# Kernel optimization log

Hardware: AMD Instinct MI355X
Metric: run time of the kernel (lower is better)

The kernel has to match this reference:

```python
import jax, jax.numpy as jnp
import numpy as np

N_ATOMS = 4096
N_EDGES = 131072
NUM_BASIS = 8
CUTOFF = 6.0
EMBED = 64      # atom embedding dim
HID = 128       # hidden channel width
SH_DIM = 9      # l=0,1,2 spherical harmonics
TP_IN = HID * SH_DIM  # 1152
N_HEADS = 4
HEAD_DIM = HID // N_HEADS


def _spherical_harmonics(vec):
    # vec: [E,3] -> [E,9] matching the torch SphericalHarmonics (l=0,1,2)
    r = jnp.linalg.norm(vec, axis=-1, keepdims=True) + 1e-8
    u = vec / r
    x, y, z = u[:, 0], u[:, 1], u[:, 2]
    l0 = jnp.ones_like(x)[:, None]
    l1 = jnp.stack([y, z, x], axis=-1)
    l2 = jnp.stack([3.0 * z * z - 1.0, x * z, y * z, x * y, x * x - y * y], axis=-1)
    return jnp.concatenate([l0, l1, l2], axis=-1)


def _rbf(d):
    # bessel RBF with cosine cutoff, d: [E] -> [E, NUM_BASIS]
    freqs = jnp.arange(1, NUM_BASIS + 1, dtype=d.dtype) * (np.pi / CUTOFF)
    cut = 0.5 * (jnp.cos(d * (np.pi / CUTOFF)) + 1.0) * (d < CUTOFF).astype(d.dtype)
    rbf = jnp.sin(d[:, None] * freqs) / d[:, None]
    return rbf * cut[:, None]


def _mace_block(atomic_numbers, edge_index, edge_vectors, edge_lengths,
                atom_embed, rad_w1, rad_b1, rad_w2, rad_b2, tp_w, tp_b,
                msg_w1, msg_b1, msg_w2, msg_b2,
                attn_w_in, attn_b_in, attn_w_out, attn_b_out,
                gate_w, gate_b, out_w, out_b):
    n_atoms = atom_embed.shape[0] if False else atomic_numbers.shape[0]
    node = atom_embed[atomic_numbers]                      # [N,64] gather
    sh = _spherical_harmonics(edge_vectors)                # [E,9]
    rbf = _rbf(edge_lengths)                               # [E,8]
    rad = jax.nn.silu(rbf @ rad_w1 + rad_b1)
    rad = jax.nn.silu(rad @ rad_w2 + rad_b2)               # [E,128]
    # per-l outer products radial x sh_l, flattened channel-major, concatenated
    slices = [(0, 1), (1, 4), (4, 9)]
    msgs = jnp.concatenate(
        [(rad[:, :, None] * sh[:, None, s:e]).reshape(rad.shape[0], -1) for s, e in slices],
        axis=-1)                                           # [E,1152]
    edge_msg = msgs @ tp_w + tp_b                          # [E,128]
    dst = edge_index[1]
    agg = jax.ops.segment_sum(edge_msg, dst, num_segments=n_atoms)  # [N,128] scatter-add
    combined = jnp.concatenate([node, agg], axis=-1)       # [N,192]
    upd = jax.nn.silu(combined @ msg_w1 + msg_b1) @ msg_w2 + msg_b2  # [N,128]
    # multi-head self-attention over all atoms (batch of 1)
    qkv = upd @ attn_w_in.T + attn_b_in                    # [N,384]
    q, k, v = jnp.split(qkv, 3, axis=-1)
    q = q.reshape(-1, N_HEADS, HEAD_DIM)
    k = k.reshape(-1, N_HEADS, HEAD_DIM)
    v = v.reshape(-1, N_HEADS, HEAD_DIM)
    scores = jnp.einsum('nhd,mhd->hnm', q, k) / np.sqrt(HEAD_DIM)
    attn = jax.nn.softmax(scores, axis=-1)
    att = jnp.einsum('hnm,mhd->nhd', attn, v).reshape(-1, HID)
    att = att @ attn_w_out.T + attn_b_out                  # [N,128]
    gate = jax.nn.sigmoid(upd @ gate_w + gate_b)
    out = gate * att + (1.0 - gate) * upd
    return out @ out_w + out_b                             # [N,128]


def setup_inputs() -> dict:
    key = jax.random.key(0)
    ks = jax.random.split(key, 20)
    def w(k, shape, s=0.05):
        return jax.random.normal(k, shape, dtype=jnp.float32) * s
    return {
        'atomic_numbers': jax.random.randint(ks[0], (N_ATOMS,), 0, 100),
        'positions': jax.random.normal(ks[1], (N_ATOMS, 3), dtype=jnp.float32),
        'edge_index': jax.random.randint(ks[2], (2, N_EDGES), 0, N_ATOMS),
        'edge_vectors': jax.random.normal(ks[3], (N_EDGES, 3), dtype=jnp.float32),
        'edge_lengths': jax.random.uniform(ks[4], (N_EDGES,), dtype=jnp.float32, minval=0.5, maxval=5.9),
        'atom_embed': w(ks[5], (100, EMBED), 1.0),
        'rad_w1': w(ks[6], (NUM_BASIS, 64)), 'rad_b1': jnp.zeros((64,), jnp.float32),
        'rad_w2': w(ks[7], (64, HID)), 'rad_b2': jnp.zeros((HID,), jnp.float32),
        'tp_w': w(ks[8], (TP_IN, HID)), 'tp_b': jnp.zeros((HID,), jnp.float32),
        'msg_w1': w(ks[9], (EMBED + HID, HID)), 'msg_b1': jnp.zeros((HID,), jnp.float32),
        'msg_w2': w(ks[10], (HID, HID)), 'msg_b2': jnp.zeros((HID,), jnp.float32),
        'attn_w_in': w(ks[11], (3 * HID, HID)), 'attn_b_in': jnp.zeros((3 * HID,), jnp.float32),
        'attn_w_out': w(ks[12], (HID, HID)), 'attn_b_out': jnp.zeros((HID,), jnp.float32),
        'gate_w': w(ks[13], (HID, HID)), 'gate_b': jnp.zeros((HID,), jnp.float32),
        'out_w': w(ks[14], (HID, HID)), 'out_b': jnp.zeros((HID,), jnp.float32),
    }


def reference(atomic_numbers, positions, edge_index, edge_vectors, edge_lengths,
              atom_embed, rad_w1, rad_b1, rad_w2, rad_b2, tp_w, tp_b,
              msg_w1, msg_b1, msg_w2, msg_b2,
              attn_w_in, attn_b_in, attn_w_out, attn_b_out,
              gate_w, gate_b, out_w, out_b):
    # positions is accepted (as in the torch signature) but unused by the block math
    del positions
    return _mace_block(atomic_numbers, edge_index, edge_vectors, edge_lengths,
                       atom_embed, rad_w1, rad_b1, rad_w2, rad_b2, tp_w, tp_b,
                       msg_w1, msg_b1, msg_w2, msg_b2,
                       attn_w_in, attn_b_in, attn_w_out, attn_b_out,
                       gate_w, gate_b, out_w, out_b)
```

## Files before the change

### kernel.cpp

```cpp
#include <hip/hip_runtime.h>
#include <math.h>

#define N_ATOMS 4096
#define N_EDGES 131072
#define PI6 0.52359877559829887f
#define CAP 128

typedef __attribute__((ext_vector_type(8))) short bf16x8;
typedef __attribute__((ext_vector_type(4))) float f32x4;

#define MFMA(A,B,C) __builtin_amdgcn_mfma_f32_16x16x32_bf16((A),(B),(C),0,0,0)

__device__ __forceinline__ float silu_f(float x){ return x / (1.f + __expf(-x)); }
__device__ __forceinline__ float sigmoid_f(float x){ return 1.f / (1.f + __expf(-x)); }
__device__ __forceinline__ unsigned int f2bf(float f){
  unsigned int u = __float_as_uint(f);
  return (u + 0x7FFFu + ((u>>16)&1u)) >> 16;
}
__device__ __forceinline__ bf16x8 ld8(const unsigned short* p){
  union { unsigned int u[4]; bf16x8 v; } r;
  const unsigned int* q = (const unsigned int*)p;
  r.u[0]=q[0]; r.u[1]=q[1]; r.u[2]=q[2]; r.u[3]=q[3];
  return r.v;
}
__device__ __forceinline__ void split_store(float v, unsigned short* ph, unsigned short* pl){
  unsigned int hb = f2bf(v);
  *ph = (unsigned short)hb;
  *pl = (unsigned short)f2bf(v - __uint_as_float(hb<<16));
}

__global__ __launch_bounds__(256) void prep_kernel(
  const float* __restrict__ attn_w_out, const float* __restrict__ rad_w2,
  const float* __restrict__ tp_w, const float* __restrict__ msg_w1,
  const float* __restrict__ msg_w2, const float* __restrict__ attn_w_in,
  float* __restrict__ wt_out, int* __restrict__ cursor,
  unsigned short* __restrict__ w2t_h, unsigned short* __restrict__ w2t_l,
  unsigned short* __restrict__ tpwT_h, unsigned short* __restrict__ tpwT_l,
  unsigned short* __restrict__ w1T_h, unsigned short* __restrict__ w1T_l,
  unsigned short* __restrict__ w2T_h, unsigned short* __restrict__ w2T_l,
  unsigned short* __restrict__ awin_h, unsigned short* __restrict__ awin_l)
{
  int idx = blockIdx.x*256 + threadIdx.x;
  if (idx < 4096) cursor[idx] = 0;
  if (idx < 16384){
    int i = idx>>7, k = idx&127;
    wt_out[k*128+i] = attn_w_out[idx];
  } else if (idx < 24576){
    int j = idx - 16384; int k = j>>7, c = j&127;
    split_store(rad_w2[k*128+c], &w2t_h[c*64+k], &w2t_l[c*64+k]);
  } else if (idx < 172032){
    int j = idx - 24576; int col = j&127, kk = j>>7;
    int jj = kk>>7, c = kk&127;
    int r = (jj==0)? c : (jj<4 ? 128 + c*3 + (jj-1) : 512 + c*5 + (jj-4));
    split_store(tp_w[r*128+col], &tpwT_h[col*1152+kk], &tpwT_l[col*1152+kk]);
  } else if (idx < 196608){
    int j = idx - 172032; int col = j&127, k = j>>7;
    split_store(msg_w1[k*128+col], &w1T_h[col*192+k], &w1T_l[col*192+k]);
  } else if (idx < 212992){
    int j = idx - 196608; int col = j&127, k = j>>7;
    split_store(msg_w2[k*128+col], &w2T_h[col*128+k], &w2T_l[col*128+k]);
  } else if (idx < 262144){
    int j = idx - 212992;
    split_store(attn_w_in[j], &awin_h[j], &awin_l[j]);
  }
}

__global__ __launch_bounds__(256) void bucket_kernel(
  const int* __restrict__ edge_index, int* __restrict__ cursor, int* __restrict__ edge_slot)
{
  int e = blockIdx.x*256 + threadIdx.x;
  if (e < N_EDGES){
    int d = edge_index[N_EDGES + e];
    int pos = atomicAdd(&cursor[d], 1);
    if (pos < CAP) edge_slot[d*CAP + pos] = e;
  }
}

__global__ __launch_bounds__(512) void edge_F_kernel(
  const float* __restrict__ edge_vectors, const float* __restrict__ edge_lengths,
  const float* __restrict__ rad_w1, const float* __restrict__ rad_b1,
  const unsigned short* __restrict__ w2t_h, const unsigned short* __restrict__ w2t_l,
  const float* __restrict__ rad_b2,
  const int* __restrict__ cursor, const int* __restrict__ edge_slot,
  unsigned short* __restrict__ Fh, unsigned short* __restrict__ Fl)
{
  const int tid = threadIdx.x;
  const int w = tid >> 6, lane = tid & 63;
  const int l15 = lane & 15, lg = lane >> 4;
  const int wm = w >> 2, wn2 = w & 3;

  __shared__ unsigned short W1h[64][36],  W1l[64][36];
  __shared__ unsigned short RBh[32][36],  RBl[32][36];
  __shared__ unsigned short SHh[16][36],  SHl[16][36];
  __shared__ unsigned short R1h[32][72],  R1l[32][72];
  __shared__ unsigned short R2h[128][36], R2l[128][36];

  bf16x8 WBh[2][2], WBl[2][2];
  #pragma unroll
  for (int nt=0; nt<2; nt++){
    int row = (wn2*2+nt)*16 + l15;
    WBh[nt][0] = ld8(&w2t_h[row*64 + lg*8]);
    WBh[nt][1] = ld8(&w2t_h[row*64 + 32 + lg*8]);
    WBl[nt][0] = ld8(&w2t_l[row*64 + lg*8]);
    WBl[nt][1] = ld8(&w2t_l[row*64 + 32 + lg*8]);
  }

  for (int i = tid; i < 2048; i += 512){
    int c = i >> 5, k = i & 31;
    float v = (k < 8) ? rad_w1[k*64 + c] : 0.f;
    split_store(v, &W1h[c][k], &W1l[c][k]);
  }
  for (int i = tid; i < 32*36; i += 512){ RBh[i/36][i%36]=0; RBl[i/36][i%36]=0; }
  for (int i = tid; i < 16*36; i += 512){ SHh[i/36][i%36]=0; SHl[i/36][i%36]=0; }

  const float b1v  = rad_b1[wn2*16 + l15];
  const float b2c0 = rad_b2[wn2*32 + l15];
  const float b2c1 = rad_b2[wn2*32 + 16 + l15];

  __syncthreads();

  for (int aa = 0; aa < 4; ++aa){
    const int a = blockIdx.x*4 + aa;
    const int deg = min(cursor[a], CAP);
    const int base = a*CAP;
    f32x4 facc = {0.f,0.f,0.f,0.f};

    for (int t0 = 0; t0 < deg; t0 += 32){
      if (tid < 256){
        int e8 = tid >> 3, k = tid & 7;
        int idx = t0 + e8;
        int eid = edge_slot[base + (idx < deg ? idx : 0)];
        float d = edge_lengths[eid];
        float cut = 0.5f*(__cosf(d*PI6)+1.f)*(d<6.f?1.f:0.f);
        float rb = __sinf(d*((float)(k+1)*PI6))/d*cut;
        split_store(rb, &RBh[e8][k], &RBl[e8][k]);
      } else {
        int e8 = (tid-256) >> 3, u = tid & 7;
        int idx = t0 + e8;
        bool val = idx < deg;
        int eid = edge_slot[base + (val ? idx : 0)];
        float vx = edge_vectors[eid*3], vy = edge_vectors[eid*3+1], vz = edge_vectors[eid*3+2];
        float rn = sqrtf(vx*vx+vy*vy+vz*vz) + 1e-8f;
        float x = vx/rn, y = vy/rn, z = vz/rn;
        float sv;
        switch(u){
          case 0: sv = 1.f; break;
          case 1: sv = y; break;
          case 2: sv = z; break;
          case 3: sv = x; break;
          case 4: sv = 3.f*z*z-1.f; break;
          case 5: sv = x*z; break;
          case 6: sv = y*z; break;
          default: sv = x*y; break;
        }
        if (!val) sv = 0.f;
        split_store(sv, &SHh[u][e8], &SHl[u][e8]);
        if (u == 0){
          float s8 = val ? (x*x - y*y) : 0.f;
          split_store(s8, &SHh[8][e8], &SHl[8][e8]);
        }
      }
      __syncthreads();

      {
        bf16x8 Ah = ld8(&RBh[wm*16 + l15][lg*8]);
        bf16x8 Al = ld8(&RBl[wm*16 + l15][lg*8]);
        bf16x8 Bh = ld8(&W1h[wn2*16 + l15][lg*8]);
        bf16x8 Bl = ld8(&W1l[wn2*16 + l15][lg*8]);
        f32x4 z = {0.f,0.f,0.f,0.f};
        z = MFMA(Ah,Bl,z); z = MFMA(Al,Bh,z); z = MFMA(Ah,Bh,z);
        #pragma unroll
        for (int r=0;r<4;r++){
          int e8 = wm*16 + lg*4 + r;
          int c  = wn2*16 + l15;
          float v = silu_f(z[r] + b1v);
          split_store(v, &R1h[e8][c], &R1l[e8][c]);
        }
      }
      __syncthreads();

      {
        bf16x8 Ah0 = ld8(&R1h[wm*16+l15][lg*8]);
        bf16x8 Ah1 = ld8(&R1h[wm*16+l15][32+lg*8]);
        bf16x8 Al0 = ld8(&R1l[wm*16+l15][lg*8]);
        bf16x8 Al1 = ld8(&R1l[wm*16+l15][32+lg*8]);
        #pragma unroll
        for (int nt=0; nt<2; nt++){
          int c16 = wn2*2 + nt;
          f32x4 z = {0.f,0.f,0.f,0.f};
          z = MFMA(Al0,WBh[nt][0],z); z = MFMA(Al1,WBh[nt][1],z);
          z = MFMA(Ah0,WBl[nt][0],z); z = MFMA(Ah1,WBl[nt][1],z);
          z = MFMA(Ah0,WBh[nt][0],z); z = MFMA(Ah1,WBh[nt][1],z);
          float bb = nt ? b2c1 : b2c0;
          #pragma unroll
          for (int r=0;r<4;r++){
            int e8 = wm*16 + lg*4 + r;
            int c  = c16*16 + l15;
            float v = silu_f(z[r] + bb);
            split_store(v, &R2h[c][e8], &R2l[c][e8]);
          }
        }
      }
      __syncthreads();

      {
        bf16x8 Ah = ld8(&R2h[w*16+l15][lg*8]);
        bf16x8 Al = ld8(&R2l[w*16+l15][lg*8]);
        bf16x8 Bh = ld8(&SHh[l15][lg*8]);
        bf16x8 Bl = ld8(&SHl[l15][lg*8]);
        facc = MFMA(Ah,Bl,facc);
        facc = MFMA(Al,Bh,facc);
        facc = MFMA(Ah,Bh,facc);
      }
      __syncthreads();
    }

    if (l15 < 9){
      #pragma unroll
      for (int r=0;r<4;r++){
        int c = w*16 + lg*4 + r;
        size_t o = (size_t)l15*(N_ATOMS*128) + (size_t)a*128 + c;
        split_store(facc[r], &Fh[o], &Fl[o]);
      }
    }
  }
}

__global__ __launch_bounds__(512) void node_kernel(
  const int* __restrict__ atomic_numbers, const float* __restrict__ atom_embed,
  const unsigned short* __restrict__ Fh, const unsigned short* __restrict__ Fl,
  const unsigned short* __restrict__ tpwT_h, const unsigned short* __restrict__ tpwT_l,
  const float* __restrict__ tp_b, const int* __restrict__ cursor,
  const unsigned short* __restrict__ w1T_h, const unsigned short* __restrict__ w1T_l,
  const float* __restrict__ msg_b1,
  const unsigned short* __restrict__ w2T_h, const unsigned short* __restrict__ w2T_l,
  const float* __restrict__ msg_b2,
  const unsigned short* __restrict__ awin_h, const unsigned short* __restrict__ awin_l,
  const float* __restrict__ attn_b_in,
  float* __restrict__ upd_out,
  unsigned short* __restrict__ Qbf, unsigned short* __restrict__ Kbf,
  unsigned short* __restrict__ Vtb)
{
  const int a0 = blockIdx.x*16, tid = threadIdx.x;
  const int w = tid>>6, lane = tid&63, l15 = lane&15, lg = lane>>4;

  __shared__ unsigned short Ch[16][200], Cl[16][200];
  __shared__ unsigned short Hh[16][136], Hl[16][136];
  __shared__ unsigned short Uh[16][136], Ul[16][136];

  for (int i=tid; i<1024; i+=512){
    int a16=i>>6, k=i&63;
    float v = atom_embed[atomic_numbers[a0+a16]*64+k];
    split_store(v, &Ch[a16][k], &Cl[a16][k]);
  }

  {
    f32x4 z = {0.f,0.f,0.f,0.f};
    for (int ch=0; ch<36; ch++){
      int k0=ch*32, j=k0>>7, c0=k0&127;
      size_t aoff = (size_t)j*(N_ATOMS*128) + (size_t)(a0+l15)*128 + c0 + lg*8;
      bf16x8 Ah=ld8(Fh+aoff), Al=ld8(Fl+aoff);
      size_t boff = (size_t)(w*16+l15)*1152 + k0 + lg*8;
      bf16x8 Bh=ld8(tpwT_h+boff), Bl=ld8(tpwT_l+boff);
      z = MFMA(Ah,Bl,z); z = MFMA(Al,Bh,z); z = MFMA(Ah,Bh,z);
    }
    int col = w*16+l15;
    float tb = tp_b[col];
    #pragma unroll
    for (int r=0;r<4;r++){
      int row = lg*4+r, arow = a0+row;
      float deg = (float)cursor[arow];
      float v = z[r] + tb*deg;
      split_store(v, &Ch[row][64+col], &Cl[row][64+col]);
    }
  }
  __syncthreads();

  {
    f32x4 z = {0.f,0.f,0.f,0.f};
    #pragma unroll
    for (int ch=0; ch<6; ch++){
      int k0=ch*32;
      bf16x8 Ah=ld8(&Ch[l15][k0+lg*8]), Al=ld8(&Cl[l15][k0+lg*8]);
      size_t boff=(size_t)(w*16+l15)*192 + k0 + lg*8;
      bf16x8 Bh=ld8(w1T_h+boff), Bl=ld8(w1T_l+boff);
      z = MFMA(Ah,Bl,z); z = MFMA(Al,Bh,z); z = MFMA(Ah,Bh,z);
    }
    int col = w*16+l15;
    float mb = msg_b1[col];
    #pragma unroll
    for (int r=0;r<4;r++){
      int row = lg*4+r;
      float v = silu_f(z[r]+mb);
      split_store(v, &Hh[row][col], &Hl[row][col]);
    }
  }
  __syncthreads();

  {
    f32x4 z = {0.f,0.f,0.f,0.f};
    #pragma unroll
    for (int ch=0; ch<4; ch++){
      int k0=ch*32;
      bf16x8 Ah=ld8(&Hh[l15][k0+lg*8]), Al=ld8(&Hl[l15][k0+lg*8]);
      size_t boff=(size_t)(w*16+l15)*128 + k0 + lg*8;
      bf16x8 Bh=ld8(w2T_h+boff), Bl=ld8(w2T_l+boff);
      z = MFMA(Ah,Bl,z); z = MFMA(Al,Bh,z); z = MFMA(Ah,Bh,z);
    }
    int col = w*16+l15;
    float mb = msg_b2[col];
    #pragma unroll
    for (int r=0;r<4;r++){
      int row = lg*4+r;
      float v = z[r]+mb;
      upd_out[(size_t)(a0+row)*128 + col] = v;
      split_store(v, &Uh[row][col], &Ul[row][col]);
    }
  }
  __syncthreads();

  #pragma unroll
  for (int t3=0; t3<3; t3++){
    f32x4 z = {0.f,0.f,0.f,0.f};
    int col = (w*3+t3)*16 + l15;
    #pragma unroll
    for (int ch=0; ch<4; ch++){
      int k0=ch*32;
      bf16x8 Ah=ld8(&Uh[l15][k0+lg*8]), Al=ld8(&Ul[l15][k0+lg*8]);
      size_t boff=(size_t)col*128 + k0 + lg*8;
      bf16x8 Bh=ld8(awin_h+boff), Bl=ld8(awin_l+boff);
      z = MFMA(Ah,Bl,z); z = MFMA(Al,Bh,z); z = MFMA(Ah,Bh,z);
    }
    float ab = attn_b_in[col];
    int p = col>>7, hh = (col>>5)&3, dd = col&31;
    #pragma unroll
    for (int r=0;r<4;r++){
      int row = a0 + lg*4 + r;
      float v = z[r]+ab;
      if (p==0)      Qbf[(size_t)hh*131072 + (size_t)row*32 + dd] =
                       (unsigned short)f2bf(v*0.17677669529663687f);
      else if (p==1) Kbf[(size_t)hh*131072 + (size_t)row*32 + dd] = (unsigned short)f2bf(v);
      else           Vtb[(size_t)hh*131072 + (size_t)dd*4096 + row] = (unsigned short)f2bf(v);
    }
  }
}

__global__ __launch_bounds__(512) void attn_kernel(
  const unsigned short* __restrict__ Qbf, const unsigned short* __restrict__ Kbf,
  const unsigned short* __restrict__ Vtb, float* __restrict__ att)
{
  const int tid = threadIdx.x;
  const int w = tid>>6, lane = tid&63, l15 = lane&15, lg = lane>>4;
  const int qjl = w>>2, ks = w&3;
  const int qj = blockIdx.x*2 + qjl;
  const int h = qj >> 8, qt = qj & 255;

  __shared__ unsigned short Ps[8][16][72];
  __shared__ float MBo[2][4][16][32];
  __shared__ float MBm[2][4][16];
  __shared__ float MBs[2][4][16];

  const unsigned short* Kb = Kbf + (size_t)h*131072;
  const unsigned short* Vb = Vtb + (size_t)h*131072;

  bf16x8 bQ = ld8(&Qbf[(size_t)h*131072 + (size_t)(qt*16+l15)*32 + lg*8]);

  float m = -3e38f, su = 0.f;
  f32x4 oacc[2] = {{0.f,0.f,0.f,0.f},{0.f,0.f,0.f,0.f}};

  for (int kt = ks*16; kt < ks*16 + 16; ++kt){
    const int k0 = kt*64;
    f32x4 s[4];
    #pragma unroll
    for (int n=0;n<4;n++){
      bf16x8 aK = ld8(&Kb[(size_t)(k0+n*16+l15)*32 + lg*8]);
      f32x4 z = {0.f,0.f,0.f,0.f};
      s[n] = MFMA(aK, bQ, z);
    }
    float tmax = s[0][0];
    #pragma unroll
    for (int n=0;n<4;n++)
      #pragma unroll
      for (int r=0;r<4;r++) tmax = fmaxf(tmax, s[n][r]);
    tmax = fmaxf(tmax, __shfl_xor(tmax,16,64));
    tmax = fmaxf(tmax, __shfl_xor(tmax,32,64));
    float mn = fmaxf(m, tmax);
    float csc = __expf(m - mn);
    m = mn;
    float psum = 0.f;
    unsigned int* prow = (unsigned int*)&Ps[w][l15][0];
    #pragma unroll
    for (int n=0;n<4;n++){
      float p0=__expf(s[n][0]-mn), p1=__expf(s[n][1]-mn);
      float p2=__expf(s[n][2]-mn), p3=__expf(s[n][3]-mn);
      psum += (p0+p1)+(p2+p3);
      prow[n*8+lg*2]   = f2bf(p0) | (f2bf(p1)<<16);
      prow[n*8+lg*2+1] = f2bf(p2) | (f2bf(p3)<<16);
    }
    psum += __shfl_xor(psum,16,64);
    psum += __shfl_xor(psum,32,64);
    su = su*csc + psum;
    float cr[4];
    #pragma unroll
    for (int r=0;r<4;r++) cr[r] = __shfl(csc, lg*4+r, 64);
    #pragma unroll
    for (int nd=0;nd<2;nd++)
      #pragma unroll
      for (int r=0;r<4;r++) oacc[nd][r] *= cr[r];
    __asm__ volatile("s_waitcnt lgkmcnt(0)" ::: "memory");
    #pragma unroll
    for (int kc=0;kc<2;kc++){
      bf16x8 aP = ld8(&Ps[w][l15][kc*32 + lg*8]);
      #pragma unroll
      for (int nd=0;nd<2;nd++){
        bf16x8 bV = ld8(&Vb[(size_t)(nd*16+l15)*4096 + k0 + kc*32 + lg*8]);
        oacc[nd] = MFMA(aP, bV, oacc[nd]);
      }
    }
  }

  if (lg==0){ MBm[qjl][ks][l15]=m; MBs[qjl][ks][l15]=su; }
  #pragma unroll
  for (int nd=0;nd<2;nd++)
    #pragma unroll
    for (int r=0;r<4;r++) MBo[qjl][ks][lg*4+r][nd*16+l15] = oacc[nd][r];
  __syncthreads();

  for (int idx = tid; idx < 1024; idx += 512){
    int qq = idx>>9, q = (idx>>5)&15, d = idx&31;
    float m0=MBm[qq][0][q], m1=MBm[qq][1][q], m2=MBm[qq][2][q], m3=MBm[qq][3][q];
    float mf = fmaxf(fmaxf(m0,m1), fmaxf(m2,m3));
    float c0=__expf(m0-mf), c1=__expf(m1-mf), c2=__expf(m2-mf), c3=__expf(m3-mf);
    float st = MBs[qq][0][q]*c0 + MBs[qq][1][q]*c1 + MBs[qq][2][q]*c2 + MBs[qq][3][q]*c3;
    float o  = MBo[qq][0][q][d]*c0 + MBo[qq][1][q][d]*c1 + MBo[qq][2][q][d]*c2 + MBo[qq][3][q][d]*c3;
    int qj2 = blockIdx.x*2 + qq;
    int hh = qj2>>8, qrow = (qj2&255)*16 + q;
    att[(size_t)qrow*128 + hh*32 + d] = o/st;
  }
}

__global__ __launch_bounds__(512) void final_kernel(
  const float* __restrict__ att, const float* __restrict__ upd,
  const float* __restrict__ wt_out, const float* __restrict__ attn_b_out,
  const float* __restrict__ gate_w, const float* __restrict__ gate_b,
  const float* __restrict__ out_w, const float* __restrict__ out_b,
  float* __restrict__ out)
{
  const int a0 = blockIdx.x*8, tid = threadIdx.x;
  const int g = tid >> 7, o = tid & 127;
  __shared__ float att_s[8][128], upd_s[8][128], tmps[8][128];
  for (int i=tid; i<1024; i+=512){
    int a8 = i>>7, k = i&127;
    att_s[a8][k] = att[(a0+a8)*128+k];
    upd_s[a8][k] = upd[(a0+a8)*128+k];
  }
  __syncthreads();
  const int aA = 2*g, aB = 2*g+1;
  float a2A = attn_b_out[o], a2B = a2A;
  float gA = gate_b[o], gB = gA;
  for (int k=0;k<128;k++){
    float wa = wt_out[k*128+o];
    float wg = gate_w[k*128+o];
    a2A += att_s[aA][k]*wa; a2B += att_s[aB][k]*wa;
    gA  += upd_s[aA][k]*wg; gB  += upd_s[aB][k]*wg;
  }
  gA = sigmoid_f(gA); gB = sigmoid_f(gB);
  tmps[aA][o] = gA*a2A + (1.f-gA)*upd_s[aA][o];
  tmps[aB][o] = gB*a2B + (1.f-gB)*upd_s[aB][o];
  __syncthreads();
  float ouA = out_b[o], ouB = ouA;
  for (int k=0;k<128;k++){
    float w = out_w[k*128+o];
    ouA += tmps[aA][k]*w; ouB += tmps[aB][k]*w;
  }
  out[(a0+aA)*128+o] = ouA;
  out[(a0+aB)*128+o] = ouB;
}

extern "C" void kernel_launch(void* const* d_in, const int* in_sizes, int n_in,
                              void* d_out, int out_size, void* d_ws, size_t ws_size,
                              hipStream_t stream){
  const int*   atomic_numbers = (const int*)  d_in[0];
  const int*   edge_index     = (const int*)  d_in[2];
  const float* edge_vectors   = (const float*)d_in[3];
  const float* edge_lengths   = (const float*)d_in[4];
  const float* atom_embed     = (const float*)d_in[5];
  const float* rad_w1 = (const float*)d_in[6];
  const float* rad_b1 = (const float*)d_in[7];
  const float* rad_w2 = (const float*)d_in[8];
  const float* rad_b2 = (const float*)d_in[9];
  const float* tp_w   = (const float*)d_in[10];
  const float* tp_b   = (const float*)d_in[11];
  const float* msg_w1 = (const float*)d_in[12];
  const float* msg_b1 = (const float*)d_in[13];
  const float* msg_w2 = (const float*)d_in[14];
  const float* msg_b2 = (const float*)d_in[15];
  const float* attn_w_in  = (const float*)d_in[16];
  const float* attn_b_in  = (const float*)d_in[17];
  const float* attn_w_out = (const float*)d_in[18];
  const float* attn_b_out = (const float*)d_in[19];
  const float* gate_w = (const float*)d_in[20];
  const float* gate_b = (const float*)d_in[21];
  const float* out_w  = (const float*)d_in[22];
  const float* out_b  = (const float*)d_in[23];

  char* ws = (char*)d_ws;
  int* cursor    = (int*)(ws);
  int* edge_slot = (int*)(ws + 16384);
  float* wt_out  = (float*)(ws + 2113536);
  unsigned short* w2t_h  = (unsigned short*)(ws + 2179072);
  unsigned short* w2t_l  = (unsigned short*)(ws + 2195456);
  unsigned short* tpwT_h = (unsigned short*)(ws + 2211840);
  unsigned short* tpwT_l = (unsigned short*)(ws + 2506752);
  unsigned short* w1T_h  = (unsigned short*)(ws + 2801664);
  unsigned short* w1T_l  = (unsigned short*)(ws + 2850816);
  unsigned short* w2T_h  = (unsigned short*)(ws + 2899968);
  unsigned short* w2T_l  = (unsigned short*)(ws + 2932736);
  unsigned short* awin_h = (unsigned short*)(ws + 2965504);
  unsigned short* awin_l = (unsigned short*)(ws + 3063808);
  unsigned short* Fbf_h  = (unsigned short*)(ws + 3162112);
  unsigned short* Fbf_l  = (unsigned short*)(ws + 12599296);
  float* att     = (float*)(ws + 3162112);
  float* upd     = (float*)(ws + 22036480);
  unsigned short* Qbf = (unsigned short*)(ws + 24133632);
  unsigned short* Kbf = (unsigned short*)(ws + 25182208);
  unsigned short* Vtb = (unsigned short*)(ws + 26230784);

  prep_kernel<<<1024, 256, 0, stream>>>(attn_w_out, rad_w2, tp_w, msg_w1, msg_w2, attn_w_in,
      wt_out, cursor, w2t_h, w2t_l, tpwT_h, tpwT_l, w1T_h, w1T_l, w2T_h, w2T_l, awin_h, awin_l);
  bucket_kernel<<<(N_EDGES+255)/256, 256, 0, stream>>>(edge_index, cursor, edge_slot);
  edge_F_kernel<<<N_ATOMS/4, 512, 0, stream>>>(edge_vectors, edge_lengths,
      rad_w1, rad_b1, w2t_h, w2t_l, rad_b2, cursor, edge_slot, Fbf_h, Fbf_l);
  node_kernel<<<N_ATOMS/16, 512, 0, stream>>>(atomic_numbers, atom_embed,
      Fbf_h, Fbf_l, tpwT_h, tpwT_l, tp_b, cursor,
      w1T_h, w1T_l, msg_b1, w2T_h, w2T_l, msg_b2, awin_h, awin_l, attn_b_in,
      upd, Qbf, Kbf, Vtb);
  attn_kernel<<<512, 512, 0, stream>>>(Qbf, Kbf, Vtb, att);
  final_kernel<<<N_ATOMS/8, 512, 0, stream>>>(att, upd, wt_out, attn_b_out,
      gate_w, gate_b, out_w, out_b, (float*)d_out);
}
```

Before: 191.9 us.

## Process 64-edge tiles and keep layer-2 output per-wave to drop a barrier

The edge tile grows from 32 to 64 edges, and every thread now computes both RBF and spherical-harmonic values instead of splitting that work across halves. The layer-2 GEMM is transposed so each wave owns 16 output channels and writes them to a private per-wave LDS buffer. The SH contraction then reads that buffer after only a wave-local waitcnt, which removes one block-wide __syncthreads per tile and halves the number of tile iterations. In exchange the kernel uses more LDS and registers, and atoms with low degree waste more work on padding rows.

```diff
diff --git a/kernel.cpp b/kernel.cpp
--- a/kernel.cpp
+++ b/kernel.cpp
@@ -87,35 +87,36 @@
   const int tid = threadIdx.x;
   const int w = tid >> 6, lane = tid & 63;
   const int l15 = lane & 15, lg = lane >> 4;
-  const int wm = w >> 2, wn2 = w & 3;
+  const int m = w >> 1, nh = w & 1;
 
   __shared__ unsigned short W1h[64][36],  W1l[64][36];
-  __shared__ unsigned short RBh[32][36],  RBl[32][36];
-  __shared__ unsigned short SHh[16][36],  SHl[16][36];
-  __shared__ unsigned short R1h[32][72],  R1l[32][72];
-  __shared__ unsigned short R2h[128][36], R2l[128][36];
-
-  bf16x8 WBh[2][2], WBl[2][2];
-  #pragma unroll
-  for (int nt=0; nt<2; nt++){
-    int row = (wn2*2+nt)*16 + l15;
-    WBh[nt][0] = ld8(&w2t_h[row*64 + lg*8]);
-    WBh[nt][1] = ld8(&w2t_h[row*64 + 32 + lg*8]);
-    WBl[nt][0] = ld8(&w2t_l[row*64 + lg*8]);
-    WBl[nt][1] = ld8(&w2t_l[row*64 + 32 + lg*8]);
-  }
-
-  for (int i = tid; i < 2048; i += 512){
-    int c = i >> 5, k = i & 31;
+  __shared__ unsigned short RBh[64][36],  RBl[64][36];
+  __shared__ unsigned short SHh[16][72],  SHl[16][72];
+  __shared__ unsigned short R1h[64][66],  R1l[64][66];
+  __shared__ unsigned short R2wh[8][16][34], R2wl[8][16][34];
+
+  bf16x8 WAh[2], WAl[2];
+  {
+    int c = w*16 + l15;
+    WAh[0] = ld8(&w2t_h[c*64 + lg*8]);
+    WAh[1] = ld8(&w2t_h[c*64 + 32 + lg*8]);
+    WAl[0] = ld8(&w2t_l[c*64 + lg*8]);
+    WAl[1] = ld8(&w2t_l[c*64 + 32 + lg*8]);
+  }
+
+  for (int i = tid; i < 64*36; i += 512){
+    int c = i/36, k = i%36;
     float v = (k < 8) ? rad_w1[k*64 + c] : 0.f;
     split_store(v, &W1h[c][k], &W1l[c][k]);
-  }
-  for (int i = tid; i < 32*36; i += 512){ RBh[i/36][i%36]=0; RBl[i/36][i%36]=0; }
-  for (int i = tid; i < 16*36; i += 512){ SHh[i/36][i%36]=0; SHl[i/36][i%36]=0; }
-
-  const float b1v  = rad_b1[wn2*16 + l15];
-  const float b2c0 = rad_b2[wn2*32 + l15];
-  const float b2c1 = rad_b2[wn2*32 + 16 + l15];
+    RBh[c][k]=0; RBl[c][k]=0;
+  }
+  for (int i = tid; i < 16*72; i += 512){ SHh[i/72][i%72]=0; SHl[i/72][i%72]=0; }
+
+  const float b1A = rad_b1[nh*32 + l15];
+  const float b1B = rad_b1[nh*32 + 16 + l15];
+  float b2r[4];
+  #pragma unroll
+  for (int r=0;r<4;r++) b2r[r] = rad_b2[w*16 + lg*4 + r];
 
   __syncthreads();
 
@@ -125,20 +126,16 @@
     const int base = a*CAP;
     f32x4 facc = {0.f,0.f,0.f,0.f};
 
-    for (int t0 = 0; t0 < deg; t0 += 32){
-      if (tid < 256){
-        int e8 = tid >> 3, k = tid & 7;
-        int idx = t0 + e8;
-        int eid = edge_slot[base + (idx < deg ? idx : 0)];
-        float d = edge_lengths[eid];
-        float cut = 0.5f*(__cosf(d*PI6)+1.f)*(d<6.f?1.f:0.f);
-        float rb = __sinf(d*((float)(k+1)*PI6))/d*cut;
-        split_store(rb, &RBh[e8][k], &RBl[e8][k]);
-      } else {
-        int e8 = (tid-256) >> 3, u = tid & 7;
+    for (int t0 = 0; t0 < deg; t0 += 64){
+      {
+        int e8 = tid >> 3, u = tid & 7;
         int idx = t0 + e8;
         bool val = idx < deg;
         int eid = edge_slot[base + (val ? idx : 0)];
+        float d = edge_lengths[eid];
+        float cut = 0.5f*(__cosf(d*PI6)+1.f)*(d<6.f?1.f:0.f);
+        float rb = __sinf(d*((float)(u+1)*PI6))/d*cut;
+        split_store(rb, &RBh[e8][u], &RBl[e8][u]);
         float vx = edge_vectors[eid*3], vy = edge_vectors[eid*3+1], vz = edge_vectors[eid*3+2];
         float rn = sqrtf(vx*vx+vy*vy+vz*vz) + 1e-8f;
         float x = vx/rn, y = vy/rn, z = vz/rn;
@@ -163,54 +160,56 @@
       __syncthreads();
 
       {
-        bf16x8 Ah = ld8(&RBh[wm*16 + l15][lg*8]);
-        bf16x8 Al = ld8(&RBl[wm*16 + l15][lg*8]);
-        bf16x8 Bh = ld8(&W1h[wn2*16 + l15][lg*8]);
-        bf16x8 Bl = ld8(&W1l[wn2*16 + l15][lg*8]);
-        f32x4 z = {0.f,0.f,0.f,0.f};
-        z = MFMA(Ah,Bl,z); z = MFMA(Al,Bh,z); z = MFMA(Ah,Bh,z);
-        #pragma unroll
-        for (int r=0;r<4;r++){
-          int e8 = wm*16 + lg*4 + r;
-          int c  = wn2*16 + l15;
-          float v = silu_f(z[r] + b1v);
-          split_store(v, &R1h[e8][c], &R1l[e8][c]);
-        }
-      }
-      __syncthreads();
-
-      {
-        bf16x8 Ah0 = ld8(&R1h[wm*16+l15][lg*8]);
-        bf16x8 Ah1 = ld8(&R1h[wm*16+l15][32+lg*8]);
-        bf16x8 Al0 = ld8(&R1l[wm*16+l15][lg*8]);
-        bf16x8 Al1 = ld8(&R1l[wm*16+l15][32+lg*8]);
+        bf16x8 Ah = ld8(&RBh[m*16 + l15][lg*8]);
+        bf16x8 Al = ld8(&RBl[m*16 + l15][lg*8]);
         #pragma unroll
         for (int nt=0; nt<2; nt++){
-          int c16 = wn2*2 + nt;
+          int c = nh*32 + nt*16 + l15;
+          bf16x8 Bh = ld8(&W1h[c][lg*8]);
+          bf16x8 Bl = ld8(&W1l[c][lg*8]);
           f32x4 z = {0.f,0.f,0.f,0.f};
-          z = MFMA(Al0,WBh[nt][0],z); z = MFMA(Al1,WBh[nt][1],z);
-          z = MFMA(Ah0,WBl[nt][0],z); z = MFMA(Ah1,WBl[nt][1],z);
-          z = MFMA(Ah0,WBh[nt][0],z); z = MFMA(Ah1,WBh[nt][1],z);
-          float bb = nt ? b2c1 : b2c0;
+          z = MFMA(Ah,Bl,z); z = MFMA(Al,Bh,z); z = MFMA(Ah,Bh,z);
+          float bb = nt ? b1B : b1A;
           #pragma unroll
           for (int r=0;r<4;r++){
-            int e8 = wm*16 + lg*4 + r;
-            int c  = c16*16 + l15;
+            int e8 = m*16 + lg*4 + r;
+            int cc = nh*32 + nt*16 + l15;
             float v = silu_f(z[r] + bb);
-            split_store(v, &R2h[c][e8], &R2l[c][e8]);
+            split_store(v, &R1h[e8][cc], &R1l[e8][cc]);
           }
         }
       }
       __syncthreads();
 
-      {
-        bf16x8 Ah = ld8(&R2h[w*16+l15][lg*8]);
-        bf16x8 Al = ld8(&R2l[w*16+l15][lg*8]);
-        bf16x8 Bh = ld8(&SHh[l15][lg*8]);
-        bf16x8 Bl = ld8(&SHl[l15][lg*8]);
-        facc = MFMA(Ah,Bl,facc);
-        facc = MFMA(Al,Bh,facc);
-        facc = MFMA(Ah,Bh,facc);
+      #pragma unroll
+      for (int eh=0; eh<2; eh++){
+        #pragma unroll
+        for (int nt2=0; nt2<2; nt2++){
+          int et = eh*2 + nt2;
+          bf16x8 Bh0 = ld8(&R1h[et*16+l15][lg*8]);
+          bf16x8 Bh1 = ld8(&R1h[et*16+l15][32+lg*8]);
+          bf16x8 Bl0 = ld8(&R1l[et*16+l15][lg*8]);
+          bf16x8 Bl1 = ld8(&R1l[et*16+l15][32+lg*8]);
+          f32x4 z = {0.f,0.f,0.f,0.f};
+          z = MFMA(WAl[0],Bh0,z); z = MFMA(WAl[1],Bh1,z);
+          z = MFMA(WAh[0],Bl0,z); z = MFMA(WAh[1],Bl1,z);
+          z = MFMA(WAh[0],Bh0,z); z = MFMA(WAh[1],Bh1,z);
+          #pragma unroll
+          for (int r=0;r<4;r++){
+            float v = silu_f(z[r] + b2r[r]);
+            split_store(v, &R2wh[w][lg*4+r][nt2*16+l15], &R2wl[w][lg*4+r][nt2*16+l15]);
+          }
+        }
+        __asm__ volatile("s_waitcnt lgkmcnt(0)" ::: "memory");
+        {
+          bf16x8 Ah = ld8(&R2wh[w][l15][lg*8]);
+          bf16x8 Al = ld8(&R2wl[w][l15][lg*8]);
+          bf16x8 Bh = ld8(&SHh[l15][eh*32 + lg*8]);
+          bf16x8 Bl = ld8(&SHl[l15][eh*32 + lg*8]);
+          facc = MFMA(Ah,Bl,facc);
+          facc = MFMA(Al,Bh,facc);
+          facc = MFMA(Ah,Bh,facc);
+        }
       }
       __syncthreads();
     }
```

New measurement: 192.4 us. No clear change (+0.2%).

## Make second radial layer wave-local to drop a block barrier

Applied to the files above, without the earlier changes.

Each wave now computes its own 16-channel slice of the second radial MLP layer across all 32 edges, with W2 transposed as the A operand. The result goes to a per-wave LDS buffer, so the following tensor-product MFMA only needs a wave-local lgkmcnt wait instead of a block-wide __syncthreads. Padded RBF rows are zeroed explicitly so that invalid edges contribute nothing. The scheme relies on wave-local LDS ordering and on the sched_barrier being placed correctly.

```diff
diff --git a/kernel.cpp b/kernel.cpp
--- a/kernel.cpp
+++ b/kernel.cpp
@@ -93,16 +93,15 @@
   __shared__ unsigned short RBh[32][36],  RBl[32][36];
   __shared__ unsigned short SHh[16][36],  SHl[16][36];
   __shared__ unsigned short R1h[32][72],  R1l[32][72];
-  __shared__ unsigned short R2h[128][36], R2l[128][36];
-
-  bf16x8 WBh[2][2], WBl[2][2];
-  #pragma unroll
-  for (int nt=0; nt<2; nt++){
-    int row = (wn2*2+nt)*16 + l15;
-    WBh[nt][0] = ld8(&w2t_h[row*64 + lg*8]);
-    WBh[nt][1] = ld8(&w2t_h[row*64 + 32 + lg*8]);
-    WBl[nt][0] = ld8(&w2t_l[row*64 + lg*8]);
-    WBl[nt][1] = ld8(&w2t_l[row*64 + 32 + lg*8]);
+  __shared__ unsigned short R2wh[8][16][34], R2wl[8][16][34];
+
+  bf16x8 WAh[2], WAl[2];
+  {
+    int c = w*16 + l15;
+    WAh[0] = ld8(&w2t_h[c*64 + lg*8]);
+    WAh[1] = ld8(&w2t_h[c*64 + 32 + lg*8]);
+    WAl[0] = ld8(&w2t_l[c*64 + lg*8]);
+    WAl[1] = ld8(&w2t_l[c*64 + 32 + lg*8]);
   }
 
   for (int i = tid; i < 2048; i += 512){
@@ -113,9 +112,10 @@
   for (int i = tid; i < 32*36; i += 512){ RBh[i/36][i%36]=0; RBl[i/36][i%36]=0; }
   for (int i = tid; i < 16*36; i += 512){ SHh[i/36][i%36]=0; SHl[i/36][i%36]=0; }
 
-  const float b1v  = rad_b1[wn2*16 + l15];
-  const float b2c0 = rad_b2[wn2*32 + l15];
-  const float b2c1 = rad_b2[wn2*32 + 16 + l15];
+  const float b1v = rad_b1[wn2*16 + l15];
+  float b2r[4];
+  #pragma unroll
+  for (int r=0;r<4;r++) b2r[r] = rad_b2[w*16 + lg*4 + r];
 
   __syncthreads();
 
@@ -133,6 +133,7 @@
         float d = edge_lengths[eid];
         float cut = 0.5f*(__cosf(d*PI6)+1.f)*(d<6.f?1.f:0.f);
         float rb = __sinf(d*((float)(k+1)*PI6))/d*cut;
+        if (idx >= deg) rb = 0.f;
         split_store(rb, &RBh[e8][k], &RBl[e8][k]);
       } else {
         int e8 = (tid-256) >> 3, u = tid & 7;
@@ -179,33 +180,27 @@
       }
       __syncthreads();
 
-      {
-        bf16x8 Ah0 = ld8(&R1h[wm*16+l15][lg*8]);
-        bf16x8 Ah1 = ld8(&R1h[wm*16+l15][32+lg*8]);
-        bf16x8 Al0 = ld8(&R1l[wm*16+l15][lg*8]);
-        bf16x8 Al1 = ld8(&R1l[wm*16+l15][32+lg*8]);
+      #pragma unroll
+      for (int et=0; et<2; et++){
+        bf16x8 Bh0 = ld8(&R1h[et*16+l15][lg*8]);
+        bf16x8 Bh1 = ld8(&R1h[et*16+l15][32+lg*8]);
+        bf16x8 Bl0 = ld8(&R1l[et*16+l15][lg*8]);
+        bf16x8 Bl1 = ld8(&R1l[et*16+l15][32+lg*8]);
+        f32x4 z = {0.f,0.f,0.f,0.f};
+        z = MFMA(WAl[0],Bh0,z); z = MFMA(WAl[1],Bh1,z);
+        z = MFMA(WAh[0],Bl0,z); z = MFMA(WAh[1],Bl1,z);
+        z = MFMA(WAh[0],Bh0,z); z = MFMA(WAh[1],Bh1,z);
         #pragma unroll
-        for (int nt=0; nt<2; nt++){
-          int c16 = wn2*2 + nt;
-          f32x4 z = {0.f,0.f,0.f,0.f};
-          z = MFMA(Al0,WBh[nt][0],z); z = MFMA(Al1,WBh[nt][1],z);
-          z = MFMA(Ah0,WBl[nt][0],z); z = MFMA(Ah1,WBl[nt][1],z);
-          z = MFMA(Ah0,WBh[nt][0],z); z = MFMA(Ah1,WBh[nt][1],z);
-          float bb = nt ? b2c1 : b2c0;
-          #pragma unroll
-          for (int r=0;r<4;r++){
-            int e8 = wm*16 + lg*4 + r;
-            int c  = c16*16 + l15;
-            float v = silu_f(z[r] + bb);
-            split_store(v, &R2h[c][e8], &R2l[c][e8]);
-          }
+        for (int r=0;r<4;r++){
+          float v = silu_f(z[r] + b2r[r]);
+          split_store(v, &R2wh[w][lg*4+r][et*16+l15], &R2wl[w][lg*4+r][et*16+l15]);
         }
       }
-      __syncthreads();
-
+      __asm__ volatile("s_waitcnt lgkmcnt(0)" ::: "memory");
+      __builtin_amdgcn_sched_barrier(0);
       {
-        bf16x8 Ah = ld8(&R2h[w*16+l15][lg*8]);
-        bf16x8 Al = ld8(&R2l[w*16+l15][lg*8]);
+        bf16x8 Ah = ld8(&R2wh[w][l15][lg*8]);
+        bf16x8 Al = ld8(&R2wl[w][l15][lg*8]);
         bf16x8 Bh = ld8(&SHh[l15][lg*8]);
         bf16x8 Bl = ld8(&SHl[l15][lg*8]);
         facc = MFMA(Ah,Bl,facc);
```

Measured after the change: 185.2 us. 1.04x faster.
